# Optimization experiments

Measured on AMD Instinct MI355X. Metric: run time of the kernel, lower is better.

Reference implementation:

```python
import jax, jax.numpy as jnp
import numpy as np

ALPHA = 0.2          # LeakyReLU negative slope
NEG_BIG = -9e15      # mask fill value from the original code
N, IN_F, OUT_F = 8192, 128, 64


def setup_inputs() -> dict:
    key = jax.random.key(0)
    k1, k2, k3, k4 = jax.random.split(key, 4)
    h = jax.random.normal(k1, (N, IN_F), dtype=jnp.float32)
    adj = jax.random.randint(k2, (N, N), 0, 2, dtype=jnp.int32)
    W = jax.random.normal(k3, (IN_F, OUT_F), dtype=jnp.float32) * 0.1
    a = jax.random.normal(k4, (2 * OUT_F, 1), dtype=jnp.float32) * 0.1
    return {"h": h, "adj": adj, "W": W, "a": a}


def reference(h, adj, W, a):
    # Wh: [N, F]
    Wh = h @ W
    # e_ij = leakyrelu([Wh_i ; Wh_j] . a) = leakyrelu(Wh_i.a1 + Wh_j.a2)
    # (identical math to the original NxNx2F concat, without materializing it)
    a1 = a[:OUT_F, 0]   # [F]
    a2 = a[OUT_F:, 0]   # [F]
    s1 = Wh @ a1        # [N]
    s2 = Wh @ a2        # [N]
    e = jax.nn.leaky_relu(s1[:, None] + s2[None, :], negative_slope=ALPHA)  # [N, N]
    e = jnp.where(adj > 0, e, jnp.float32(NEG_BIG))
    attention = jax.nn.softmax(e, axis=1)
    # dropout is identity at inference (training=False)
    h_prime = attention @ Wh  # [N, F]
    return jax.nn.elu(h_prime)  # concat=True -> elu
```

## Files before the change

### kernel.cpp

```cpp
#include <hip/hip_runtime.h>
#include <hip/hip_bf16.h>

#define N 8192
#define IN_F 128
#define OUT_F 64
#define LRELU_ALPHA 0.2f

typedef __attribute__((ext_vector_type(8))) short short8;
typedef __attribute__((ext_vector_type(4))) float float4v;
typedef __attribute__((ext_vector_type(4))) unsigned short ushortx4;

__device__ __forceinline__ unsigned short bf16_bits(float x) {
  unsigned u = __builtin_bit_cast(unsigned, x);
  u += 0x7fffu + ((u >> 16) & 1u);
  return (unsigned short)(u >> 16);
}

__global__ __launch_bounds__(256) void prep_kernel(
    const float* __restrict__ h, const float* __restrict__ W,
    const float* __restrict__ a, float* __restrict__ s1,
    float* __restrict__ s2, unsigned short* __restrict__ whT) {
  const int tid = threadIdx.x;
  const int row = blockIdx.x * 4 + (tid >> 6);
  const int k = tid & 63;
  const float* hr = h + row * IN_F;
  float acc = 0.f;
#pragma unroll 8
  for (int c = 0; c < IN_F; ++c) acc = fmaf(hr[c], W[c * OUT_F + k], acc);
  whT[(long)k * N + row] = bf16_bits(acc);
  float p1 = acc * a[k];
  float p2 = acc * a[OUT_F + k];
#pragma unroll
  for (int off = 32; off > 0; off >>= 1) {
    p1 += __shfl_xor(p1, off);
    p2 += __shfl_xor(p2, off);
  }
  if (k == 0) { s1[row] = p1; s2[row] = p2; }
}

__global__ __launch_bounds__(256) void repack_kernel(
    const unsigned short* __restrict__ whT, unsigned short* __restrict__ whF) {
  const int f = blockIdx.x * 256 + threadIdx.x;
  const int lane = f & 63, tt = (f >> 6) & 3, c = f >> 8;
  const int r16 = lane & 15, quad = lane >> 4;
  const short8 v = *(const short8*)(whT + (long)(tt * 16 + r16) * N + c * 32 + quad * 8);
  *(short8*)(whF + (long)f * 8) = v;
}

#define PSTR 264
#define WREG (16 * PSTR * 2)

__global__ __launch_bounds__(512, 4) void gat_kernel(
    const int* __restrict__ adj, const float* __restrict__ s1,
    const float* __restrict__ s2, const unsigned short* __restrict__ whF,
    float* __restrict__ out) {
  __shared__ __align__(16) unsigned char lds_raw[8 * WREG];
  const int tid = threadIdx.x;
  const int w = tid >> 6, L = tid & 63;
  const int r16 = L & 15, quad = L >> 4;
  const int row0 = blockIdx.x * 16;
  unsigned short* pl = (unsigned short*)(lds_raw + w * WREG);

  float s1r[16];
#pragma unroll
  for (int r = 0; r < 16; ++r) s1r[r] = s1[row0 + r];

  float4v acc0 = {0.f, 0.f, 0.f, 0.f};
  float4v acc1 = {0.f, 0.f, 0.f, 0.f};
  float4v acc2 = {0.f, 0.f, 0.f, 0.f};
  float4v acc3 = {0.f, 0.f, 0.f, 0.f};
  float4v accL = {0.f, 0.f, 0.f, 0.f};
  const short ONE = (short)0x3F80;
  const short8 ones = {ONE, ONE, ONE, ONE, ONE, ONE, ONE, ONE};

  for (int s = 0; s < 4; ++s) {
    const int col = w * 1024 + s * 256 + L * 4;
    const float4 s2v = *(const float4*)(s2 + col);
    int4 av[16];
#pragma unroll
    for (int r = 0; r < 16; ++r)
      av[r] = *(const int4*)(adj + (long)(row0 + r) * N + col);
#pragma unroll
    for (int r = 0; r < 16; ++r) {
      float e0 = s1r[r] + s2v.x; e0 = fmaxf(e0, LRELU_ALPHA * e0);
      float e1 = s1r[r] + s2v.y; e1 = fmaxf(e1, LRELU_ALPHA * e1);
      float e2 = s1r[r] + s2v.z; e2 = fmaxf(e2, LRELU_ALPHA * e2);
      float e3 = s1r[r] + s2v.w; e3 = fmaxf(e3, LRELU_ALPHA * e3);
      const float p0 = av[r].x > 0 ? __expf(e0) : 0.f;
      const float p1 = av[r].y > 0 ? __expf(e1) : 0.f;
      const float p2 = av[r].z > 0 ? __expf(e2) : 0.f;
      const float p3 = av[r].w > 0 ? __expf(e3) : 0.f;
      ushortx4 pk = {bf16_bits(p0), bf16_bits(p1), bf16_bits(p2), bf16_bits(p3)};
      *(ushortx4*)(pl + r * PSTR + L * 4) = pk;
    }
#pragma unroll
    for (int sub = 0; sub < 8; ++sub) {
      const short8 afrag = *(const short8*)(pl + r16 * PSTR + sub * 32 + quad * 8);
      const int c32 = w * 32 + s * 8 + sub;
      const unsigned short* bp = whF + ((long)c32 * 4 * 64 + L) * 8;
      const short8 b0 = *(const short8*)(bp + 0 * 512);
      const short8 b1 = *(const short8*)(bp + 1 * 512);
      const short8 b2 = *(const short8*)(bp + 2 * 512);
      const short8 b3 = *(const short8*)(bp + 3 * 512);
      acc0 = __builtin_amdgcn_mfma_f32_16x16x32_bf16(afrag, b0, acc0, 0, 0, 0);
      acc1 = __builtin_amdgcn_mfma_f32_16x16x32_bf16(afrag, b1, acc1, 0, 0, 0);
      acc2 = __builtin_amdgcn_mfma_f32_16x16x32_bf16(afrag, b2, acc2, 0, 0, 0);
      acc3 = __builtin_amdgcn_mfma_f32_16x16x32_bf16(afrag, b3, acc3, 0, 0, 0);
      accL = __builtin_amdgcn_mfma_f32_16x16x32_bf16(afrag, ones, accL, 0, 0, 0);
    }
  }

  float* F = (float*)pl;
#pragma unroll
  for (int reg = 0; reg < 4; ++reg) {
    const int r = quad * 4 + reg;
    F[r * 65 + 0 * 16 + r16] = acc0[reg];
    F[r * 65 + 1 * 16 + r16] = acc1[reg];
    F[r * 65 + 2 * 16 + r16] = acc2[reg];
    F[r * 65 + 3 * 16 + r16] = acc3[reg];
    if (r16 == 0) F[1040 + r] = accL[reg];
  }
  __syncthreads();

  for (int o = tid; o < 16 * 64; o += 512) {
    const int r = o >> 6, k = o & 63;
    float S = 0.f, Lx = 0.f;
#pragma unroll
    for (int ww = 0; ww < 8; ++ww) {
      const float* Fw = (const float*)(lds_raw + ww * WREG);
      S += Fw[r * 65 + k];
      Lx += Fw[1040 + r];
    }
    const float v = S / Lx;
    out[(long)(row0 + r) * OUT_F + k] = v > 0.f ? v : expm1f(v);
  }
}

extern "C" void kernel_launch(void* const* d_in, const int* in_sizes, int n_in,
                              void* d_out, int out_size, void* d_ws, size_t ws_size,
                              hipStream_t stream) {
  const float* h = (const float*)d_in[0];
  const int* adj = (const int*)d_in[1];
  const float* W = (const float*)d_in[2];
  const float* a = (const float*)d_in[3];
  float* out = (float*)d_out;

  float* s1 = (float*)d_ws;
  float* s2 = s1 + N;
  unsigned short* whT = (unsigned short*)(s2 + N);
  unsigned short* whF = whT + (long)OUT_F * N;

  prep_kernel<<<N / 4, 256, 0, stream>>>(h, W, a, s1, s2, whT);
  repack_kernel<<<N * OUT_F / 8 / 256, 256, 0, stream>>>(whT, whF);
  gat_kernel<<<N / 16, 512, 0, stream>>>(adj, s1, s2, whF, out);
}
```

Before: 423.8 us.

## Restructure GAT kernel into 16-wave double-buffered row-per-wave pipeline

Each block now runs 16 waves, and each wave computes the attention probabilities for a single adjacency row across a 512-column chunk into a shared double-buffered LDS tile. All waves then consume the tile via MFMA on their own 32-column slice. The next chunk's adj and s2 loads are issued before the MFMA work so memory latency overlaps compute. The cost is a block-wide barrier per iteration. The final reduction is reworked to merge 16 wave partials in two phases. The aim is to cut per-thread register pressure (no 16-row adj array) and raise memory-level parallelism on the bandwidth-bound adjacency stream.

```diff
diff --git a/kernel.cpp b/kernel.cpp
--- a/kernel.cpp
+++ b/kernel.cpp
@@ -5,6 +5,7 @@
 #define IN_F 128
 #define OUT_F 64
 #define LRELU_ALPHA 0.2f
+#define PAD 520
 
 typedef __attribute__((ext_vector_type(8))) short short8;
 typedef __attribute__((ext_vector_type(4))) float float4v;
@@ -47,91 +48,119 @@
   *(short8*)(whF + (long)f * 8) = v;
 }
 
-#define PSTR 264
-#define WREG (16 * PSTR * 2)
+__device__ __forceinline__ void p_write(unsigned short* pr, int c, int4 av,
+                                        float4 s2v, float s1w) {
+  float e0 = s1w + s2v.x; e0 = fmaxf(e0, LRELU_ALPHA * e0);
+  float e1 = s1w + s2v.y; e1 = fmaxf(e1, LRELU_ALPHA * e1);
+  float e2 = s1w + s2v.z; e2 = fmaxf(e2, LRELU_ALPHA * e2);
+  float e3 = s1w + s2v.w; e3 = fmaxf(e3, LRELU_ALPHA * e3);
+  const float p0 = av.x > 0 ? __expf(e0) : 0.f;
+  const float p1 = av.y > 0 ? __expf(e1) : 0.f;
+  const float p2 = av.z > 0 ? __expf(e2) : 0.f;
+  const float p3 = av.w > 0 ? __expf(e3) : 0.f;
+  ushortx4 pk = {bf16_bits(p0), bf16_bits(p1), bf16_bits(p2), bf16_bits(p3)};
+  *(ushortx4*)(pr + c) = pk;
+}
 
-__global__ __launch_bounds__(512, 4) void gat_kernel(
+__global__ __launch_bounds__(1024, 4) void gat_kernel(
     const int* __restrict__ adj, const float* __restrict__ s1,
     const float* __restrict__ s2, const unsigned short* __restrict__ whF,
     float* __restrict__ out) {
-  __shared__ __align__(16) unsigned char lds_raw[8 * WREG];
+  __shared__ __align__(16) unsigned short pbuf[2][16][PAD];
   const int tid = threadIdx.x;
   const int w = tid >> 6, L = tid & 63;
   const int r16 = L & 15, quad = L >> 4;
   const int row0 = blockIdx.x * 16;
-  unsigned short* pl = (unsigned short*)(lds_raw + w * WREG);
-
-  float s1r[16];
-#pragma unroll
-  for (int r = 0; r < 16; ++r) s1r[r] = s1[row0 + r];
+  const long arow = (long)(row0 + w) * N;
+  const float s1w = s1[row0 + w];
 
   float4v acc0 = {0.f, 0.f, 0.f, 0.f};
   float4v acc1 = {0.f, 0.f, 0.f, 0.f};
   float4v acc2 = {0.f, 0.f, 0.f, 0.f};
   float4v acc3 = {0.f, 0.f, 0.f, 0.f};
-  float4v accL = {0.f, 0.f, 0.f, 0.f};
+  float4v accD = {0.f, 0.f, 0.f, 0.f};
   const short ONE = (short)0x3F80;
   const short8 ones = {ONE, ONE, ONE, ONE, ONE, ONE, ONE, ONE};
 
-  for (int s = 0; s < 4; ++s) {
-    const int col = w * 1024 + s * 256 + L * 4;
-    const float4 s2v = *(const float4*)(s2 + col);
-    int4 av[16];
-#pragma unroll
-    for (int r = 0; r < 16; ++r)
-      av[r] = *(const int4*)(adj + (long)(row0 + r) * N + col);
-#pragma unroll
-    for (int r = 0; r < 16; ++r) {
-      float e0 = s1r[r] + s2v.x; e0 = fmaxf(e0, LRELU_ALPHA * e0);
-      float e1 = s1r[r] + s2v.y; e1 = fmaxf(e1, LRELU_ALPHA * e1);
-      float e2 = s1r[r] + s2v.z; e2 = fmaxf(e2, LRELU_ALPHA * e2);
-      float e3 = s1r[r] + s2v.w; e3 = fmaxf(e3, LRELU_ALPHA * e3);
-      const float p0 = av[r].x > 0 ? __expf(e0) : 0.f;
-      const float p1 = av[r].y > 0 ? __expf(e1) : 0.f;
-      const float p2 = av[r].z > 0 ? __expf(e2) : 0.f;
-      const float p3 = av[r].w > 0 ? __expf(e3) : 0.f;
-      ushortx4 pk = {bf16_bits(p0), bf16_bits(p1), bf16_bits(p2), bf16_bits(p3)};
-      *(ushortx4*)(pl + r * PSTR + L * 4) = pk;
-    }
-#pragma unroll
-    for (int sub = 0; sub < 8; ++sub) {
-      const short8 afrag = *(const short8*)(pl + r16 * PSTR + sub * 32 + quad * 8);
-      const int c32 = w * 32 + s * 8 + sub;
-      const unsigned short* bp = whF + ((long)c32 * 4 * 64 + L) * 8;
-      const short8 b0 = *(const short8*)(bp + 0 * 512);
-      const short8 b1 = *(const short8*)(bp + 1 * 512);
-      const short8 b2 = *(const short8*)(bp + 2 * 512);
-      const short8 b3 = *(const short8*)(bp + 3 * 512);
-      acc0 = __builtin_amdgcn_mfma_f32_16x16x32_bf16(afrag, b0, acc0, 0, 0, 0);
-      acc1 = __builtin_amdgcn_mfma_f32_16x16x32_bf16(afrag, b1, acc1, 0, 0, 0);
-      acc2 = __builtin_amdgcn_mfma_f32_16x16x32_bf16(afrag, b2, acc2, 0, 0, 0);
-      acc3 = __builtin_amdgcn_mfma_f32_16x16x32_bf16(afrag, b3, acc3, 0, 0, 0);
-      accL = __builtin_amdgcn_mfma_f32_16x16x32_bf16(afrag, ones, accL, 0, 0, 0);
-    }
-  }
-
-  float* F = (float*)pl;
-#pragma unroll
-  for (int reg = 0; reg < 4; ++reg) {
-    const int r = quad * 4 + reg;
-    F[r * 65 + 0 * 16 + r16] = acc0[reg];
-    F[r * 65 + 1 * 16 + r16] = acc1[reg];
-    F[r * 65 + 2 * 16 + r16] = acc2[reg];
-    F[r * 65 + 3 * 16 + r16] = acc3[reg];
-    if (r16 == 0) F[1040 + r] = accL[reg];
+  {
+    const int c = L * 4;
+    const int4 a0 = *(const int4*)(adj + arow + c);
+    const int4 a1 = *(const int4*)(adj + arow + 256 + c);
+    const float4 sv0 = *(const float4*)(s2 + c);
+    const float4 sv1 = *(const float4*)(s2 + 256 + c);
+    p_write(pbuf[0][w], c, a0, sv0, s1w);
+    p_write(pbuf[0][w], 256 + c, a1, sv1, s1w);
   }
   __syncthreads();
 
-  for (int o = tid; o < 16 * 64; o += 512) {
-    const int r = o >> 6, k = o & 63;
-    float S = 0.f, Lx = 0.f;
+  for (int it = 0; it < 16; ++it) {
+    const int b = it & 1;
+    int4 na0, na1;
+    float4 ns0, ns1;
+    if (it < 15) {
+      const long base = arow + (it + 1) * 512 + L * 4;
+      na0 = *(const int4*)(adj + base);
+      na1 = *(const int4*)(adj + base + 256);
+      ns0 = *(const float4*)(s2 + (it + 1) * 512 + L * 4);
+      ns1 = *(const float4*)(s2 + (it + 1) * 512 + 256 + L * 4);
+    }
+    const int c32 = it * 16 + w;
+    const short8 afrag = *(const short8*)(&pbuf[b][r16][w * 32 + quad * 8]);
+    const unsigned short* bp = whF + ((long)c32 * 256 + L) * 8;
+    const short8 b0 = *(const short8*)(bp);
+    const short8 b1 = *(const short8*)(bp + 512);
+    const short8 b2 = *(const short8*)(bp + 1024);
+    const short8 b3 = *(const short8*)(bp + 1536);
+    acc0 = __builtin_amdgcn_mfma_f32_16x16x32_bf16(afrag, b0, acc0, 0, 0, 0);
+    acc1 = __builtin_amdgcn_mfma_f32_16x16x32_bf16(afrag, b1, acc1, 0, 0, 0);
+    acc2 = __builtin_amdgcn_mfma_f32_16x16x32_bf16(afrag, b2, acc2, 0, 0, 0);
+    acc3 = __builtin_amdgcn_mfma_f32_16x16x32_bf16(afrag, b3, acc3, 0, 0, 0);
+    accD = __builtin_amdgcn_mfma_f32_16x16x32_bf16(afrag, ones, accD, 0, 0, 0);
+    if (it < 15) {
+      unsigned short* pr = pbuf[b ^ 1][w];
+      const int c = L * 4;
+      p_write(pr, c, na0, ns0, s1w);
+      p_write(pr, 256 + c, na1, ns1, s1w);
+    }
+    __syncthreads();
+  }
+
+  float* M = (float*)pbuf;
+  if (w >= 8) {
+    float* S = M + (w - 8) * 1040;
 #pragma unroll
-    for (int ww = 0; ww < 8; ++ww) {
-      const float* Fw = (const float*)(lds_raw + ww * WREG);
-      S += Fw[r * 65 + k];
-      Lx += Fw[1040 + r];
+    for (int reg = 0; reg < 4; ++reg) {
+      const int r = quad * 4 + reg;
+      S[r * 64 + 0 * 16 + r16] = acc0[reg];
+      S[r * 64 + 1 * 16 + r16] = acc1[reg];
+      S[r * 64 + 2 * 16 + r16] = acc2[reg];
+      S[r * 64 + 3 * 16 + r16] = acc3[reg];
+      if (r16 == 0) S[1024 + r] = accD[reg];
     }
-    const float v = S / Lx;
+  }
+  __syncthreads();
+  if (w < 8) {
+    float* S = M + w * 1040;
+#pragma unroll
+    for (int reg = 0; reg < 4; ++reg) {
+      const int r = quad * 4 + reg;
+      S[r * 64 + 0 * 16 + r16] += acc0[reg];
+      S[r * 64 + 1 * 16 + r16] += acc1[reg];
+      S[r * 64 + 2 * 16 + r16] += acc2[reg];
+      S[r * 64 + 3 * 16 + r16] += acc3[reg];
+      if (r16 == 0) S[1024 + r] += accD[reg];
+    }
+  }
+  __syncthreads();
+  {
+    const int r = tid >> 6, k = tid & 63;
+    float Sv = 0.f, Lv = 0.f;
+#pragma unroll
+    for (int s = 0; s < 8; ++s) {
+      Sv += M[s * 1040 + r * 64 + k];
+      Lv += M[s * 1040 + 1024 + r];
+    }
+    const float v = Sv / Lv;
     out[(long)(row0 + r) * OUT_F + k] = v > 0.f ? v : expm1f(v);
   }
 }
@@ -152,5 +181,5 @@
 
   prep_kernel<<<N / 4, 256, 0, stream>>>(h, W, a, s1, s2, whT);
   repack_kernel<<<N * OUT_F / 8 / 256, 256, 0, stream>>>(whT, whF);
-  gat_kernel<<<N / 16, 512, 0, stream>>>(adj, s1, s2, whF, out);
+  gat_kernel<<<N / 16, 1024, 0, stream>>>(adj, s1, s2, whF, out);
 }
```

Result: faster. 391.1 us (-7.7%).

## Split fused attention kernel into score-materialization and MFMA aggregation kernels

Applied to the files above, without the earlier changes.

The fused kernel, which computed masked exp scores into LDS and then ran MFMA against Wh, is split in two. A new pscore kernel streams the int32 adjacency, writes bf16 probabilities in MFMA fragment layout to a global N×N workspace, and uses a 2D grid for more parallelism. A separate pv kernel loads those fragments directly into MFMA operands with no LDS staging. This adds a 128MB bf16 write plus a 128MB read on top of the 256MB adjacency read, in exchange for removing the LDS round trip and improving occupancy and streaming in each phase.

```diff
diff --git a/kernel.cpp b/kernel.cpp
--- a/kernel.cpp
+++ b/kernel.cpp
@@ -8,7 +8,6 @@
 
 typedef __attribute__((ext_vector_type(8))) short short8;
 typedef __attribute__((ext_vector_type(4))) float float4v;
-typedef __attribute__((ext_vector_type(4))) unsigned short ushortx4;
 
 __device__ __forceinline__ unsigned short bf16_bits(float x) {
   unsigned u = __builtin_bit_cast(unsigned, x);
@@ -47,78 +46,81 @@
   *(short8*)(whF + (long)f * 8) = v;
 }
 
-#define PSTR 264
-#define WREG (16 * PSTR * 2)
+__global__ __launch_bounds__(256) void pscore_kernel(
+    const int* __restrict__ adj, const float* __restrict__ s1,
+    const float* __restrict__ s2, unsigned short* __restrict__ pfrag) {
+  const int tid = threadIdx.x;
+  const int w = tid >> 6, L = tid & 63;
+  const int rt = blockIdx.x, cs = blockIdx.y;
+  const int row0 = rt * 16;
+  const int j0 = cs * 2048 + w * 512 + L * 8;
+  const float4 sv0 = *(const float4*)(s2 + j0);
+  const float4 sv1 = *(const float4*)(s2 + j0 + 4);
+  const int c = j0 >> 5, quad = (j0 >> 3) & 3;
+  unsigned short* dst = pfrag + ((long)(rt * 256 + c) * 64 + quad * 16) * 8;
+#pragma unroll
+  for (int r = 0; r < 16; ++r) {
+    const int4* ap = (const int4*)(adj + (long)(row0 + r) * N + j0);
+    const int4 a0 = ap[0], a1 = ap[1];
+    const float s1w = s1[row0 + r];
+    float e[8];
+    e[0] = s1w + sv0.x; e[1] = s1w + sv0.y; e[2] = s1w + sv0.z; e[3] = s1w + sv0.w;
+    e[4] = s1w + sv1.x; e[5] = s1w + sv1.y; e[6] = s1w + sv1.z; e[7] = s1w + sv1.w;
+    const int am[8] = {a0.x, a0.y, a0.z, a0.w, a1.x, a1.y, a1.z, a1.w};
+    short8 pk;
+#pragma unroll
+    for (int i = 0; i < 8; ++i) {
+      float t = fmaxf(e[i], LRELU_ALPHA * e[i]);
+      const float p = am[i] > 0 ? __expf(t) : 0.f;
+      pk[i] = (short)bf16_bits(p);
+    }
+    *(short8*)(dst + r * 8) = pk;
+  }
+}
 
-__global__ __launch_bounds__(512, 4) void gat_kernel(
-    const int* __restrict__ adj, const float* __restrict__ s1,
-    const float* __restrict__ s2, const unsigned short* __restrict__ whF,
-    float* __restrict__ out) {
-  __shared__ __align__(16) unsigned char lds_raw[8 * WREG];
+__global__ __launch_bounds__(512) void pv_kernel(
+    const unsigned short* __restrict__ pfrag,
+    const unsigned short* __restrict__ whF, float* __restrict__ out) {
+  __shared__ float lds_acc[8][16][65];
+  __shared__ float lds_l[8][16];
   const int tid = threadIdx.x;
   const int w = tid >> 6, L = tid & 63;
   const int r16 = L & 15, quad = L >> 4;
-  const int row0 = blockIdx.x * 16;
-  unsigned short* pl = (unsigned short*)(lds_raw + w * WREG);
-
-  float s1r[16];
-#pragma unroll
-  for (int r = 0; r < 16; ++r) s1r[r] = s1[row0 + r];
+  const int rt = blockIdx.x, row0 = rt * 16;
 
   float4v acc0 = {0.f, 0.f, 0.f, 0.f};
   float4v acc1 = {0.f, 0.f, 0.f, 0.f};
   float4v acc2 = {0.f, 0.f, 0.f, 0.f};
   float4v acc3 = {0.f, 0.f, 0.f, 0.f};
-  float4v accL = {0.f, 0.f, 0.f, 0.f};
+  float4v accD = {0.f, 0.f, 0.f, 0.f};
   const short ONE = (short)0x3F80;
   const short8 ones = {ONE, ONE, ONE, ONE, ONE, ONE, ONE, ONE};
 
-  for (int s = 0; s < 4; ++s) {
-    const int col = w * 1024 + s * 256 + L * 4;
-    const float4 s2v = *(const float4*)(s2 + col);
-    int4 av[16];
-#pragma unroll
-    for (int r = 0; r < 16; ++r)
-      av[r] = *(const int4*)(adj + (long)(row0 + r) * N + col);
-#pragma unroll
-    for (int r = 0; r < 16; ++r) {
-      float e0 = s1r[r] + s2v.x; e0 = fmaxf(e0, LRELU_ALPHA * e0);
-      float e1 = s1r[r] + s2v.y; e1 = fmaxf(e1, LRELU_ALPHA * e1);
-      float e2 = s1r[r] + s2v.z; e2 = fmaxf(e2, LRELU_ALPHA * e2);
-      float e3 = s1r[r] + s2v.w; e3 = fmaxf(e3, LRELU_ALPHA * e3);
-      const float p0 = av[r].x > 0 ? __expf(e0) : 0.f;
-      const float p1 = av[r].y > 0 ? __expf(e1) : 0.f;
-      const float p2 = av[r].z > 0 ? __expf(e2) : 0.f;
-      const float p3 = av[r].w > 0 ? __expf(e3) : 0.f;
-      ushortx4 pk = {bf16_bits(p0), bf16_bits(p1), bf16_bits(p2), bf16_bits(p3)};
-      *(ushortx4*)(pl + r * PSTR + L * 4) = pk;
-    }
-#pragma unroll
-    for (int sub = 0; sub < 8; ++sub) {
-      const short8 afrag = *(const short8*)(pl + r16 * PSTR + sub * 32 + quad * 8);
-      const int c32 = w * 32 + s * 8 + sub;
-      const unsigned short* bp = whF + ((long)c32 * 4 * 64 + L) * 8;
-      const short8 b0 = *(const short8*)(bp + 0 * 512);
-      const short8 b1 = *(const short8*)(bp + 1 * 512);
-      const short8 b2 = *(const short8*)(bp + 2 * 512);
-      const short8 b3 = *(const short8*)(bp + 3 * 512);
-      acc0 = __builtin_amdgcn_mfma_f32_16x16x32_bf16(afrag, b0, acc0, 0, 0, 0);
-      acc1 = __builtin_amdgcn_mfma_f32_16x16x32_bf16(afrag, b1, acc1, 0, 0, 0);
-      acc2 = __builtin_amdgcn_mfma_f32_16x16x32_bf16(afrag, b2, acc2, 0, 0, 0);
-      acc3 = __builtin_amdgcn_mfma_f32_16x16x32_bf16(afrag, b3, acc3, 0, 0, 0);
-      accL = __builtin_amdgcn_mfma_f32_16x16x32_bf16(afrag, ones, accL, 0, 0, 0);
-    }
+  const unsigned short* ap = pfrag + ((long)(rt * 256 + w * 32) * 64 + L) * 8;
+  const unsigned short* bp0 = whF + ((long)(w * 32) * 256 + L) * 8;
+#pragma unroll 4
+  for (int cc = 0; cc < 32; ++cc) {
+    const short8 afrag = *(const short8*)(ap + (long)cc * 512);
+    const unsigned short* bp = bp0 + (long)cc * 2048;
+    const short8 b0 = *(const short8*)(bp);
+    const short8 b1 = *(const short8*)(bp + 512);
+    const short8 b2 = *(const short8*)(bp + 1024);
+    const short8 b3 = *(const short8*)(bp + 1536);
+    acc0 = __builtin_amdgcn_mfma_f32_16x16x32_bf16(afrag, b0, acc0, 0, 0, 0);
+    acc1 = __builtin_amdgcn_mfma_f32_16x16x32_bf16(afrag, b1, acc1, 0, 0, 0);
+    acc2 = __builtin_amdgcn_mfma_f32_16x16x32_bf16(afrag, b2, acc2, 0, 0, 0);
+    acc3 = __builtin_amdgcn_mfma_f32_16x16x32_bf16(afrag, b3, acc3, 0, 0, 0);
+    accD = __builtin_amdgcn_mfma_f32_16x16x32_bf16(afrag, ones, accD, 0, 0, 0);
   }
 
-  float* F = (float*)pl;
 #pragma unroll
   for (int reg = 0; reg < 4; ++reg) {
     const int r = quad * 4 + reg;
-    F[r * 65 + 0 * 16 + r16] = acc0[reg];
-    F[r * 65 + 1 * 16 + r16] = acc1[reg];
-    F[r * 65 + 2 * 16 + r16] = acc2[reg];
-    F[r * 65 + 3 * 16 + r16] = acc3[reg];
-    if (r16 == 0) F[1040 + r] = accL[reg];
+    lds_acc[w][r][0 * 16 + r16] = acc0[reg];
+    lds_acc[w][r][1 * 16 + r16] = acc1[reg];
+    lds_acc[w][r][2 * 16 + r16] = acc2[reg];
+    lds_acc[w][r][3 * 16 + r16] = acc3[reg];
+    if (r16 == 0) lds_l[w][r] = accD[reg];
   }
   __syncthreads();
 
@@ -126,10 +128,9 @@
     const int r = o >> 6, k = o & 63;
     float S = 0.f, Lx = 0.f;
 #pragma unroll
-    for (int ww = 0; ww < 8; ++ww) {
-      const float* Fw = (const float*)(lds_raw + ww * WREG);
-      S += Fw[r * 65 + k];
-      Lx += Fw[1040 + r];
+    for (int s = 0; s < 8; ++s) {
+      S += lds_acc[s][r][k];
+      Lx += lds_l[s][r];
     }
     const float v = S / Lx;
     out[(long)(row0 + r) * OUT_F + k] = v > 0.f ? v : expm1f(v);
@@ -149,8 +150,10 @@
   float* s2 = s1 + N;
   unsigned short* whT = (unsigned short*)(s2 + N);
   unsigned short* whF = whT + (long)OUT_F * N;
+  unsigned short* pfrag = whF + (long)OUT_F * N;
 
   prep_kernel<<<N / 4, 256, 0, stream>>>(h, W, a, s1, s2, whT);
   repack_kernel<<<N * OUT_F / 8 / 256, 256, 0, stream>>>(whT, whF);
-  gat_kernel<<<N / 16, 512, 0, stream>>>(adj, s1, s2, whF, out);
+  pscore_kernel<<<dim3(N / 16, 4), 256, 0, stream>>>(adj, s1, s2, pfrag);
+  pv_kernel<<<N / 16, 512, 0, stream>>>(pfrag, whF, out);
 }
```

Result: slower. 521.9 us (+23.2%).
